# Kernel optimization log

Measured on AMD Instinct MI355X. Metric: run time of the kernel, lower is better.

The kernel has to match this reference:

```python
import jax, jax.numpy as jnp
import numpy as np

HEADS = 4

def cnorm(x):
    # WithBias_LayerNorm over channel dim (no learnable params in source)
    mu = jnp.mean(x, axis=1, keepdims=True)
    var = jnp.mean((x - mu) ** 2, axis=1, keepdims=True)
    return (x - mu) / jnp.sqrt(var + 1e-5)

def conv1x1(x, w):  # w: (O, C)
    return jnp.einsum('bchw,oc->bohw', x, w)

def dwconv(x, w, pad, dil):
    return jax.lax.conv_general_dilated(
        x, w, (1, 1), [(pad, pad), (pad, pad)], rhs_dilation=(dil, dil),
        dimension_numbers=('NCHW', 'OIHW', 'NCHW'), feature_group_count=x.shape[1])

def pshuffle(x, r=2):  # (b, c*r^2, h, w) -> (b, c, h*r, w*r)
    b, c, h, w = x.shape
    x = x.reshape(b, c // (r * r), r, r, h, w)
    return x.transpose(0, 1, 4, 2, 5, 3).reshape(b, c // (r * r), h * r, w * r)

def punshuffle(x, r=2):  # inverse of pshuffle
    b, c, h, w = x.shape
    x = x.reshape(b, c, h // r, r, w // r, r)
    return x.transpose(0, 1, 3, 5, 2, 4).reshape(b, c * r * r, h // r, w // r)

def l2n(x):  # F.normalize over last dim
    return x / jnp.maximum(jnp.linalg.norm(x, axis=-1, keepdims=True), 1e-12)

def setup_inputs() -> dict:
    key = jax.random.key(0)
    ks = jax.random.split(key, 16)
    B, D, H, W = 2, 192, 128, 128
    HID = 512
    s = 0.02
    return {
        'F_raw': jax.random.normal(ks[0], (B, D, H, W), jnp.float32),
        'F_Y': jax.random.normal(ks[1], (B, D, H, W), jnp.float32),
        'temperature': jnp.ones((HEADS, 1, 1), jnp.float32),
        'w_raw_kv': jax.random.normal(ks[2], (2 * D, D), jnp.float32) * s,
        'w_raw_q': jax.random.normal(ks[3], (D, D), jnp.float32) * s,
        'w_rgb_kv': jax.random.normal(ks[4], (2 * D, D), jnp.float32) * s,
        'w_rgb_q': jax.random.normal(ks[5], (D, D), jnp.float32) * s,
        'w_g1': jax.random.normal(ks[6], (4 * D, 2 * D), jnp.float32) * s,
        'b_g1': jnp.zeros((4 * D,), jnp.float32),
        'w_g2': jax.random.normal(ks[7], (1, 4 * D), jnp.float32) * s,
        'b_g2': jnp.zeros((1,), jnp.float32),
        'w_fc': jax.random.normal(ks[8], (D, D), jnp.float32) * s,
        'b_fc': jnp.zeros((D,), jnp.float32),
        'w_pin': jax.random.normal(ks[9], (2 * HID, D), jnp.float32) * s,
        'w_dw5': jax.random.normal(ks[10], (HID // 4, 1, 5, 5), jnp.float32) * s,
        'w_dwd': jax.random.normal(ks[11], (HID // 4, 1, 3, 3), jnp.float32) * s,
        'w_pout': jax.random.normal(ks[12], (D, HID), jnp.float32) * s,
    }

def reference(F_raw, F_Y, temperature, w_raw_kv, w_raw_q, w_rgb_kv, w_rgb_q,
              w_g1, b_g1, w_g2, b_g2, w_fc, b_fc, w_pin, w_dw5, w_dwd, w_pout):
    Fr = cnorm(F_raw)   # source applies norm_g1 to both inputs
    Fy = cnorm(F_Y)
    b, c, h, w = Fr.shape
    hw, ch = h * w, c // HEADS

    raw_k, raw_v = jnp.split(conv1x1(Fr, w_raw_kv), 2, axis=1)
    raw_q = conv1x1(Fr, w_raw_q)
    rgb_k, rgb_v = jnp.split(conv1x1(Fy, w_rgb_kv), 2, axis=1)
    rgb_q = conv1x1(Fy, w_rgb_q)

    heads = lambda x: x.reshape(b, HEADS, ch, hw)
    raw_q, raw_k, raw_v = heads(raw_q), heads(raw_k), heads(raw_v)
    rgb_q, rgb_k, rgb_v = heads(rgb_q), heads(rgb_k), heads(rgb_v)
    raw_q, raw_k = l2n(raw_q), l2n(raw_k)
    rgb_q, rgb_k = l2n(rgb_q), l2n(rgb_k)

    attn_raw = jax.nn.softmax(jnp.einsum('bhcn,bhdn->bhcd', rgb_q, raw_k) * temperature, axis=-1)
    attn_rgb = jax.nn.softmax(jnp.einsum('bhcn,bhdn->bhcd', raw_q, rgb_k) * temperature, axis=-1)
    out_raw = jnp.einsum('bhcd,bhdn->bhcn', attn_raw, raw_v)
    out_rgb = jnp.einsum('bhcd,bhdn->bhcn', attn_rgb, rgb_v)

    fused = jnp.concatenate([Fr, Fy], axis=1)
    g = jax.nn.gelu(conv1x1(fused, w_g1) + b_g1[None, :, None, None], approximate=False)
    alpha = jax.nn.sigmoid(conv1x1(g, w_g2) + b_g2[None, :, None, None])  # (b,1,h,w)
    alpha = alpha.reshape(b, 1, 1, hw)

    context = (alpha * out_raw + (1.0 - alpha) * out_rgb).reshape(b, c, h, w)
    out = conv1x1(context, w_fc) + b_fc[None, :, None, None] + Fr + Fy

    # FeedForward
    x = conv1x1(cnorm(out), w_pin)        # (b, 2*hid, h, w)
    x = pshuffle(x)                       # (b, hid/2, 2h, 2w)
    x1, x2 = jnp.split(x, 2, axis=1)      # (b, hid/4, 2h, 2w) each
    x1 = dwconv(x1, w_dw5, pad=2, dil=1)
    x2 = dwconv(x2, w_dwd, pad=2, dil=2)
    x = (x2 * jnp.tanh(jax.nn.softplus(x2))) * x1  # mish(x2) * x1
    x = punshuffle(x)                     # (b, hid, h, w)
    return out + conv1x1(x, w_pout)
```

## Files before the change

kernel.cpp:

```cpp
#include <hip/hip_runtime.h>
#include <cstdint>
#include <cstddef>


typedef _Float16 f16;
using half8  = __attribute__((ext_vector_type(8))) _Float16;
using float4v = __attribute__((ext_vector_type(4))) float;

#define HW    16384
#define NPIX  32768

union U4H8 { uint4 u; f16 h[8]; };
union U2H4 { uint2 u; f16 h[4]; };

struct WConvArgs { const float* src[7]; f16* dst[7]; int n[7]; };
__global__ __launch_bounds__(256) void wconv_kernel(WConvArgs a) {
  int t = blockIdx.y;
  const float* s = a.src[t]; f16* d = a.dst[t]; int n = a.n[t];
  for (int i = blockIdx.x * 256 + threadIdx.x; i < n; i += gridDim.x * 256)
    d[i] = (f16)s[i];
}

__global__ __launch_bounds__(256) void cnorm_in_kernel(const float* __restrict__ x,
                                                       f16* __restrict__ fcat, int zoff) {
  __shared__ float tile[64][193];
  __shared__ float rsum[64][4], rsq[64][4], mm[64], rr[64];
  int tid = threadIdx.x;
  int P0 = blockIdx.x * 64;
  int b  = P0 >> 14;
  int p0 = P0 & (HW - 1);
  for (int i = tid; i < 64 * 192; i += 256) {
    int c = i >> 6, pp = i & 63;
    tile[pp][c] = x[((size_t)(b * 192 + c)) * HW + p0 + pp];
  }
  __syncthreads();
  {
    int pp = tid >> 2, q = tid & 3;
    float s = 0.f, s2 = 0.f;
    for (int c = q * 48; c < q * 48 + 48; c++) { float v = tile[pp][c]; s += v; s2 += v * v; }
    rsum[pp][q] = s; rsq[pp][q] = s2;
  }
  __syncthreads();
  if (tid < 64) {
    float s  = rsum[tid][0] + rsum[tid][1] + rsum[tid][2] + rsum[tid][3];
    float s2 = rsq[tid][0] + rsq[tid][1] + rsq[tid][2] + rsq[tid][3];
    float mu = s * (1.f / 192.f);
    float var = s2 * (1.f / 192.f) - mu * mu;
    mm[tid] = mu; rr[tid] = rsqrtf(var + 1e-5f);
  }
  __syncthreads();
  for (int i = tid; i < 64 * 192; i += 256) {
    int pp = i / 192, c = i - pp * 192;
    float v = (tile[pp][c] - mm[pp]) * rr[pp];
    fcat[(size_t)(P0 + pp) * 384 + zoff + c] = (f16)v;
  }
}

__global__ __launch_bounds__(256) void norm_pm_kernel(const float* __restrict__ xpm,
                                                      f16* __restrict__ outn) {
  __shared__ float tile[64][193];
  __shared__ float rsum[64][4], rsq[64][4], mm[64], rr[64];
  int tid = threadIdx.x;
  int P0 = blockIdx.x * 64;
  for (int i = tid; i < 64 * 192; i += 256) {
    int pp = i / 192, c = i - pp * 192;
    tile[pp][c] = xpm[(size_t)(P0 + pp) * 192 + c];
  }
  __syncthreads();
  {
    int pp = tid >> 2, q = tid & 3;
    float s = 0.f, s2 = 0.f;
    for (int c = q * 48; c < q * 48 + 48; c++) { float v = tile[pp][c]; s += v; s2 += v * v; }
    rsum[pp][q] = s; rsq[pp][q] = s2;
  }
  __syncthreads();
  if (tid < 64) {
    float s  = rsum[tid][0] + rsum[tid][1] + rsum[tid][2] + rsum[tid][3];
    float s2 = rsq[tid][0] + rsq[tid][1] + rsq[tid][2] + rsq[tid][3];
    float mu = s * (1.f / 192.f);
    float var = s2 * (1.f / 192.f) - mu * mu;
    mm[tid] = mu; rr[tid] = rsqrtf(var + 1e-5f);
  }
  __syncthreads();
  for (int i = tid; i < 64 * 192; i += 256) {
    int pp = i / 192, c = i - pp * 192;
    outn[(size_t)(P0 + pp) * 192 + c] = (f16)((tile[pp][c] - mm[pp]) * rr[pp]);
  }
}

struct G2Args {
  const f16* A; long lda; long aoff;
  const f16* B1; const f16* B2; int b1rows; int Nout; int K; long bStride;
  f16* outH; long ldo;
  const float* bfc; const f16* fcat; float* outpm;
  const float* bg1; const float* wg2; float* alpha_acc;
  const f16* vraw; const f16* vrgb; const float* alpha_pre; const float* bg2;
  const float* outpm_r; float* dout;
};

#define GEMM_SMEM_BYTES 33280

template <int MODE>
__device__ __forceinline__ void gemm2_body(const G2Args& g, int bx, int by, char* smem) {
  f16 (*As)[64] = (f16(*)[64])smem;
  f16 (*Bs)[64] = (f16(*)[64])(smem + 16384);
  float* salpha = (float*)(smem + 32768);

  int tid = threadIdx.x;
  int P0 = by * 128;
  int n0 = bx * 128;
  int wave = tid >> 6, lane = tid & 63, l15 = lane & 15, quad = lane >> 4;
  int m_off = (wave >> 1) * 64, n_off = (wave & 1) * 64;
  int lrow = lane >> 3, loct = lane & 7;
  const f16* B1 = g.B1 + (size_t)(P0 >> 14) * g.bStride;

  f16 hsa[4], hsb[4];
  if (MODE == 2) {
    if (tid < 128) {
      float a = g.alpha_pre[P0 + tid] + g.bg2[0];
      salpha[tid] = 1.f / (1.f + __expf(-a));
    }
    __syncthreads();
#pragma unroll
    for (int i = 0; i < 4; i++) {
      float s0 = salpha[m_off + i * 16 + l15];
      hsa[i] = (f16)s0; hsb[i] = (f16)(1.f - s0);
    }
  }

  float4v acc[4][4];
#pragma unroll
  for (int i = 0; i < 4; i++)
#pragma unroll
    for (int j = 0; j < 4; j++) acc[i][j] = (float4v){0.f, 0.f, 0.f, 0.f};

  int nkt = g.K >> 6;
  for (int kt = 0; kt < nkt; kt++) {
    int k0 = kt << 6;
#pragma unroll
    for (int j = 0; j < 4; j++) {
      int rbase = wave * 32 + j * 8;
      int r = rbase + lrow;
      int oct = loct ^ (r & 7);
      const f16* ga;
      if (MODE == 2) {
        const f16* base = (k0 < 192) ? (g.vraw + 192 + k0) : (g.vrgb + k0);
        ga = base + (size_t)(P0 + r) * 576 + oct * 8;
      } else {
        ga = g.A + (size_t)(P0 + r) * g.lda + g.aoff + k0 + oct * 8;
      }
      __builtin_amdgcn_global_load_lds((const __attribute__((address_space(1))) void*)ga,
                                       (__attribute__((address_space(3))) void*)&As[rbase][0],
                                       16, 0, 0);
    }
#pragma unroll
    for (int j = 0; j < 4; j++) {
      int rbase = wave * 32 + j * 8;
      int r = rbase + lrow;
      int oct = loct ^ (r & 7);
      int n = n0 + r;
      int nc = (n >= g.Nout) ? (g.Nout - 1) : n;
      const f16* gb = (nc < g.b1rows)
                          ? (B1 + (size_t)nc * g.K + k0 + oct * 8)
                          : (g.B2 + (size_t)(nc - g.b1rows) * g.K + k0 + oct * 8);
      __builtin_amdgcn_global_load_lds((const __attribute__((address_space(1))) void*)gb,
                                       (__attribute__((address_space(3))) void*)&Bs[rbase][0],
                                       16, 0, 0);
    }
    __syncthreads();
#pragma unroll
    for (int ks = 0; ks < 2; ks++) {
      half8 af[4], bf[4];
#pragma unroll
      for (int i = 0; i < 4; i++) {
        int ra = m_off + i * 16 + l15;
        af[i] = *(const half8*)&As[ra][(((ks * 4 + quad) ^ (l15 & 7))) * 8];
        int rb = n_off + i * 16 + l15;
        bf[i] = *(const half8*)&Bs[rb][(((ks * 4 + quad) ^ (l15 & 7))) * 8];
      }
      if (MODE == 2) {
#pragma unroll
        for (int i = 0; i < 4; i++) {
          f16 s = (k0 < 192) ? hsa[i] : hsb[i];
          half8 sv = {s, s, s, s, s, s, s, s};
          af[i] *= sv;
        }
      }
#pragma unroll
      for (int mi = 0; mi < 4; mi++)
#pragma unroll
        for (int ni = 0; ni < 4; ni++)
          acc[mi][ni] = __builtin_amdgcn_mfma_f32_16x16x32_f16(af[mi], bf[ni], acc[mi][ni], 0, 0, 0);
    }
    __syncthreads();
  }

  if (MODE == 0) {
#pragma unroll
    for (int mi = 0; mi < 4; mi++) {
      int row = P0 + m_off + mi * 16 + quad * 4;
#pragma unroll
      for (int ni = 0; ni < 4; ni++) {
        int gcol = n0 + n_off + ni * 16 + l15;
        if (gcol < g.Nout) {
#pragma unroll
          for (int r = 0; r < 4; r++)
            g.outH[(size_t)(row + r) * g.ldo + gcol] = (f16)acc[mi][ni][r];
        }
      }
    }
  } else if (MODE == 1) {
    float bg[4], wg[4];
#pragma unroll
    for (int ni = 0; ni < 4; ni++) {
      int gcol = n0 + n_off + ni * 16 + l15;
      bg[ni] = g.bg1[gcol]; wg[ni] = g.wg2[gcol];
    }
    float psum[4][4];
#pragma unroll
    for (int mi = 0; mi < 4; mi++)
#pragma unroll
      for (int r = 0; r < 4; r++) psum[mi][r] = 0.f;
#pragma unroll
    for (int mi = 0; mi < 4; mi++)
#pragma unroll
      for (int ni = 0; ni < 4; ni++)
#pragma unroll
        for (int r = 0; r < 4; r++) {
          float xx = acc[mi][ni][r] + bg[ni];
          float z = 0.7978845608f * (xx + 0.044715f * xx * xx * xx);
          float zc = fminf(fmaxf(z, -10.f), 10.f);
          float t = __expf(2.f * zc);
          float th = (t - 1.f) * __builtin_amdgcn_rcpf(t + 1.f);
          float ge = 0.5f * xx * (1.f + th);
          psum[mi][r] += ge * wg[ni];
        }
#pragma unroll
    for (int s = 1; s < 16; s <<= 1)
#pragma unroll
      for (int mi = 0; mi < 4; mi++)
#pragma unroll
        for (int r = 0; r < 4; r++) psum[mi][r] += __shfl_xor(psum[mi][r], s, 64);
    if (l15 == 0) {
#pragma unroll
      for (int mi = 0; mi < 4; mi++)
#pragma unroll
        for (int r = 0; r < 4; r++)
          atomicAdd(&g.alpha_acc[P0 + m_off + mi * 16 + quad * 4 + r], psum[mi][r]);
    }
  } else if (MODE == 2) {
#pragma unroll
    for (int mi = 0; mi < 4; mi++) {
      int prow = P0 + m_off + mi * 16 + quad * 4;
#pragma unroll
      for (int ni = 0; ni < 4; ni++) {
        int gcol = n0 + n_off + ni * 16 + l15;
        if (gcol < 192) {
#pragma unroll
          for (int r = 0; r < 4; r++) {
            size_t P = (size_t)(prow + r);
            float v = acc[mi][ni][r] + g.bfc[gcol] +
                      (float)g.fcat[P * 384 + gcol] + (float)g.fcat[P * 384 + 192 + gcol];
            g.outpm[P * 192 + gcol] = v;
          }
        }
      }
    }
  } else {
#pragma unroll
    for (int mi = 0; mi < 4; mi++) {
      int prow = P0 + m_off + mi * 16 + quad * 4;
#pragma unroll
      for (int ni = 0; ni < 4; ni++) {
        int gcol = n0 + n_off + ni * 16 + l15;
        if (gcol < 192) {
#pragma unroll
          for (int r = 0; r < 4; r++)
            acc[mi][ni][r] += g.outpm_r[(size_t)(prow + r) * 192 + gcol];
        }
      }
    }
    float (*bounce)[129] = (float(*)[129])smem;
    for (int cg = 0; cg < 4; cg++) {
      __syncthreads();
      if ((wave & 1) == (cg >> 1)) {
#pragma unroll
        for (int nn = 0; nn < 2; nn++) {
          int ni = (cg & 1) * 2 + nn;
          int lc = nn * 16 + l15;
#pragma unroll
          for (int mi = 0; mi < 4; mi++)
#pragma unroll
            for (int r = 0; r < 4; r++)
              bounce[lc][m_off + mi * 16 + quad * 4 + r] = acc[mi][ni][r];
        }
      }
      __syncthreads();
      int c = tid >> 3, ps = (tid & 7) * 16;
      int gc = n0 + cg * 32 + c;
      if (gc < 192) {
        int b = P0 >> 14, p = (P0 & (HW - 1)) + ps;
        float* dst = g.dout + ((size_t)b * 192 + gc) * HW + p;
#pragma unroll
        for (int i = 0; i < 16; i++) dst[i] = bounce[c][ps + i];
      }
    }
  }
}

template <int MODE>
__global__ __launch_bounds__(256) void gemm2_k(G2Args g) {
  __shared__ __align__(16) char smem[GEMM_SMEM_BYTES];
  gemm2_body<MODE>(g, (int)blockIdx.y, (int)blockIdx.x, smem);
}

__global__ __launch_bounds__(256) void gemm_fused_kernel(G2Args j0, G2Args j1, G2Args j2) {
  __shared__ __align__(16) char smem[GEMM_SMEM_BYTES];
  int id = blockIdx.x;
  if (id < 1280)      gemm2_body<0>(j0, id / 256, id & 255, smem);
  else if (id < 2560) gemm2_body<0>(j1, (id - 1280) / 256, id & 255, smem);
  else                gemm2_body<1>(j2, (id - 2560) / 256, id & 255, smem);
}

__global__ __launch_bounds__(256) void qk_transpose_kernel(const f16* __restrict__ qkvR,
                                                           const f16* __restrict__ qkvG,
                                                           f16* __restrict__ qkT) {
  __shared__ f16 T[64][264];
  int tid = threadIdx.x;
  int p0 = blockIdx.x * 256;
  int g  = blockIdx.y;
  int t  = blockIdx.z >> 1, b = blockIdx.z & 1;
  const f16* src = t ? qkvG : qkvR;
  int col0 = (g < 3) ? g * 64 : g * 64 + 192;
#pragma unroll
  for (int i = 0; i < 4; i++) {
    int idx = i * 256 + tid;
    int pp = idx >> 3, c8 = (idx & 7) * 8;
    const f16* s0 = src + ((size_t)(b * HW + p0 + 2 * pp)) * 576 + col0 + c8;
    uint4 v0 = *(const uint4*)s0;
    uint4 v1 = *(const uint4*)(s0 + 576);
    const unsigned* a = (const unsigned*)&v0;
    const unsigned* c = (const unsigned*)&v1;
#pragma unroll
    for (int w = 0; w < 4; w++) {
      unsigned lo = (a[w] & 0xffffu) | (c[w] << 16);
      unsigned hi = (a[w] >> 16) | (c[w] & 0xffff0000u);
      *(unsigned*)&T[c8 + 2 * w][2 * pp]     = lo;
      *(unsigned*)&T[c8 + 2 * w + 1][2 * pp] = hi;
    }
  }
  __syncthreads();
  size_t obase = ((size_t)(t * 2 + b) * 384 + g * 64) * 16384 + p0;
#pragma unroll
  for (int i = 0; i < 8; i++) {
    int idx = i * 256 + tid;
    int row = idx >> 5, p8 = (idx & 31) * 8;
    *(uint4*)(qkT + obase + (size_t)row * 16384 + p8) = *(const uint4*)&T[row][p8];
  }
}

__global__ __launch_bounds__(256) void gram_mfma_kernel(const f16* __restrict__ qkT,
                                                        float* __restrict__ gram) {
  __shared__ __align__(16) f16 As[48][136];
  __shared__ __align__(16) f16 Bs[48][136];
  __shared__ float Gacc[48][49];
  int tid = threadIdx.x;
  int chunk = blockIdx.x;
  int h = blockIdx.y >> 1, pair = blockIdx.y & 1;
  int b = blockIdx.z;
  int tA = pair ? 0 : 1, tB = pair ? 1 : 0;
  const f16* Abase = qkT + ((size_t)(tA * 2 + b) * 384 + 192 + 48 * h) * 16384;
  const f16* Bbase = qkT + ((size_t)(tB * 2 + b) * 384 + 48 * h) * 16384;
  for (int i = tid; i < 48 * 49; i += 256) ((float*)Gacc)[i] = 0.f;
  int wave = tid >> 6, lane = tid & 63, l15 = lane & 15, quad = lane >> 4;
  float4v acc[3][3];
#pragma unroll
  for (int i = 0; i < 3; i++)
#pragma unroll
    for (int j = 0; j < 3; j++) acc[i][j] = (float4v){0.f, 0.f, 0.f, 0.f};
  float ns_acc = 0.f;
  int nrow = tid >> 1, nhalf = tid & 1;

  for (int stage = 0; stage < 8; stage++) {
    int k0 = chunk * 1024 + stage * 128;
    uint4 v[6];
#pragma unroll
    for (int i = 0; i < 6; i++) {
      int idx = i * 256 + tid;
      int row = idx >> 4, seg = (idx & 15) * 8;
      const f16* p = (row < 48) ? (Abase + (size_t)row * 16384 + k0 + seg)
                                : (Bbase + (size_t)(row - 48) * 16384 + k0 + seg);
      v[i] = *(const uint4*)p;
    }
    __syncthreads();
#pragma unroll
    for (int i = 0; i < 6; i++) {
      int idx = i * 256 + tid;
      int row = idx >> 4, seg = (idx & 15) * 8;
      f16* dst = (row < 48) ? &As[row][seg] : &Bs[row - 48][seg];
      *(uint4*)dst = v[i];
    }
    __syncthreads();
    int kk = wave * 32;
    half8 af[3], bf[3];
#pragma unroll
    for (int i = 0; i < 3; i++) {
      af[i] = *(const half8*)&As[i * 16 + l15][kk + quad * 8];
      bf[i] = *(const half8*)&Bs[i * 16 + l15][kk + quad * 8];
    }
#pragma unroll
    for (int mi = 0; mi < 3; mi++)
#pragma unroll
      for (int ni = 0; ni < 3; ni++)
        acc[mi][ni] = __builtin_amdgcn_mfma_f32_16x16x32_f16(af[mi], bf[ni], acc[mi][ni], 0, 0, 0);
    if (tid < 192) {
      const f16* r = (nrow < 48) ? &As[nrow][nhalf * 64] : &Bs[nrow - 48][nhalf * 64];
#pragma unroll
      for (int e = 0; e < 8; e++) {
        U4H8 tt; tt.u = *(const uint4*)(r + e * 8);
#pragma unroll
        for (int j = 0; j < 8; j++) { float x = (float)tt.h[j]; ns_acc += x * x; }
      }
    }
  }
  __syncthreads();
  for (int w = 0; w < 4; w++) {
    if (wave == w) {
#pragma unroll
      for (int mi = 0; mi < 3; mi++)
#pragma unroll
        for (int ni = 0; ni < 3; ni++)
#pragma unroll
          for (int r = 0; r < 4; r++)
            Gacc[mi * 16 + quad * 4 + r][ni * 16 + l15] += acc[mi][ni][r];
    }
    __syncthreads();
  }
  float* base = gram + ((size_t)b * 4 + h) * 4800;
  float* G = base + pair * 2304;
  for (int i = tid; i < 2304; i += 256)
    atomicAdd(G + i, Gacc[i / 48][i - (i / 48) * 48]);
  if (tid < 192) {
    int slot = pair * 2 + (nrow >= 48 ? 1 : 0);
    int ch = (nrow >= 48) ? (nrow - 48) : nrow;
    atomicAdd(base + 4608 + slot * 48 + ch, ns_acc);
  }
}

__global__ void softmax_kernel(const float* __restrict__ gram, const float* __restrict__ temp,
                               float* __restrict__ att) {
  int id = blockIdx.x;
  int b = id >> 3, h = (id >> 1) & 3, pr = id & 1;
  int tid = threadIdx.x;
  __shared__ float srk[48];
  const float* base = gram + ((size_t)b * 4 + h) * 4800;
  const float* G  = base + pr * 2304;
  const float* nq = base + 4608 + (pr ? 96 : 0);
  const float* nk = base + 4608 + (pr ? 144 : 48);
  if (tid < 48) srk[tid] = 1.f / fmaxf(sqrtf(nk[tid]), 1e-12f);
  __syncthreads();
  if (tid < 48) {
    float rq = 1.f / fmaxf(sqrtf(nq[tid]), 1e-12f);
    float T = temp[h];
    float s[48], mx = -1e30f;
#pragma unroll
    for (int d = 0; d < 48; d++) { s[d] = T * G[tid * 48 + d] * rq * srk[d]; mx = fmaxf(mx, s[d]); }
    float sum = 0.f;
#pragma unroll
    for (int d = 0; d < 48; d++) { s[d] = __expf(s[d] - mx); sum += s[d]; }
    float inv = 1.f / sum;
    float* A = att + (((size_t)b * 2 + pr) * 4 + h) * 2304 + tid * 48;
#pragma unroll
    for (int d = 0; d < 48; d++) A[d] = s[d] * inv;
  }
}

__global__ __launch_bounds__(256) void mbuild_kernel(const float* __restrict__ wfc,
                                                     const float* __restrict__ att,
                                                     f16* __restrict__ mcat) {
  int e = blockIdx.x * 256 + threadIdx.x;
  if (e >= 147456) return;
  int b = e / 73728, r = e - b * 73728;
  int o = r / 384, j = r - o * 384;
  int pr = j / 192, jj = j - pr * 192;
  int h = jj / 48, d = jj - h * 48;
  const float* A = att + (((size_t)b * 2 + pr) * 4 + h) * 2304 + d;
  const float* w = wfc + o * 192 + h * 48;
  float s = 0.f;
  for (int c = 0; c < 48; c++) s += w[c] * A[c * 48];
  mcat[(size_t)b * 73728 + o * 384 + j] = (f16)s;
}

__global__ __launch_bounds__(256) void dwmish_kernel(const f16* __restrict__ hid,
                                                     const float* __restrict__ w5,
                                                     const float* __restrict__ w3,
                                                     f16* __restrict__ u) {
  __shared__ f16 sx[324][8];
  int tid = threadIdx.x;
  int c = blockIdx.y, b = blockIdx.z;
  int ti0 = (blockIdx.x >> 3) * 16, tj0 = (blockIdx.x & 7) * 16;
  const float* wp5 = w5 + c * 25;
  const float* wp3 = w3 + c * 9;
  for (int pix = tid; pix < 324; pix += 256) {
    int pi = pix / 18, pj = pix - pi * 18;
    int gi = ti0 - 1 + pi, gj = tj0 - 1 + pj;
    uint2 v0 = {0u, 0u}, v1 = {0u, 0u};
    if (gi >= 0 && gi < 128 && gj >= 0 && gj < 128) {
      const f16* base = hid + ((size_t)b * HW + gi * 128 + gj) * 1024 + c * 4;
      v0 = *(const uint2*)base;
      v1 = *(const uint2*)(base + 512);
    }
    uint4 vv = {v0.x, v0.y, v1.x, v1.y};
    *(uint4*)&sx[pix][0] = vv;
  }
  __syncthreads();
  int ti = tid >> 4, tj = tid & 15;
  U4H8 px[3][3];
#pragma unroll
  for (int dy = 0; dy < 3; dy++)
#pragma unroll
    for (int dx = 0; dx < 3; dx++)
      px[dy][dx].u = *(const uint4*)&sx[(ti + dy) * 18 + tj + dx][0];
  float xf[3][3][8];
#pragma unroll
  for (int dy = 0; dy < 3; dy++)
#pragma unroll
    for (int dx = 0; dx < 3; dx++)
#pragma unroll
      for (int e = 0; e < 8; e++) xf[dy][dx][e] = (float)px[dy][dx].h[e];
  U2H4 res;
#pragma unroll
  for (int pq = 0; pq < 4; pq++) {
    int p = pq >> 1, q = pq & 1;
    float a2 = 0.f;
#pragma unroll
    for (int ky = 0; ky < 3; ky++)
#pragma unroll
      for (int kx = 0; kx < 3; kx++)
        a2 += wp3[ky * 3 + kx] * xf[ky][kx][4 + pq];
    float a1 = 0.f;
#pragma unroll
    for (int dy = -2; dy <= 2; dy++)
#pragma unroll
      for (int dx = -2; dx <= 2; dx++) {
        int s = p + dy, t2 = q + dx;
        int di = s >> 1, ps_ = s & 1;
        int dj = t2 >> 1, qs_ = t2 & 1;
        a1 += wp5[(dy + 2) * 5 + dx + 2] * xf[1 + di][1 + dj][ps_ * 2 + qs_];
      }
    float t = __expf(fminf(a2, 20.f));
    float num = t * (t + 2.f);
    float m = a2 * num * __builtin_amdgcn_rcpf(num + 2.f);
    res.h[pq] = (f16)(m * a1);
  }
  int gi = ti0 + ti, gj = tj0 + tj;
  *(uint2*)(u + ((size_t)b * HW + gi * 128 + gj) * 512 + c * 4) = res.u;
}

extern "C" void kernel_launch(void* const* d_in, const int* in_sizes, int n_in,
                              void* d_out, int out_size, void* d_ws, size_t ws_size,
                              hipStream_t stream) {
  const float* F_raw    = (const float*)d_in[0];
  const float* F_Y      = (const float*)d_in[1];
  const float* temp     = (const float*)d_in[2];
  const float* w_raw_kv = (const float*)d_in[3];
  const float* w_raw_q  = (const float*)d_in[4];
  const float* w_rgb_kv = (const float*)d_in[5];
  const float* w_rgb_q  = (const float*)d_in[6];
  const float* w_g1     = (const float*)d_in[7];
  const float* b_g1     = (const float*)d_in[8];
  const float* w_g2     = (const float*)d_in[9];
  const float* b_g2     = (const float*)d_in[10];
  const float* w_fc     = (const float*)d_in[11];
  const float* b_fc     = (const float*)d_in[12];
  const float* w_pin    = (const float*)d_in[13];
  const float* w_dw5    = (const float*)d_in[14];
  const float* w_dwd    = (const float*)d_in[15];
  const float* w_pout   = (const float*)d_in[16];
  char* ws = (char*)d_ws;
  float* dout = (float*)d_out;

  const size_t O_FCAT  = 0;
  const size_t O_QKV0  = 25165824;
  const size_t O_QKV1  = 62914560;
  const size_t O_ALPHA = 100663296;
  const size_t O_GRAM  = 100794368;
  const size_t O_ATT   = 100947968;
  const size_t O_MCAT  = 101095424;
  const size_t O_WB    = 101390336;
  const size_t O_OUTPM = 103012352;
  const size_t O_QKT   = 103012352;
  const size_t O_NORM  = 128178176;
  const size_t O_HID   = O_QKV0;
  const size_t O_U     = 140761088;
  if (ws_size < 174315520) return;

  f16* wb      = (f16*)(ws + O_WB);
  f16* wb_kvR  = wb;
  f16* wb_qR   = wb + 73728;
  f16* wb_kvG  = wb + 110592;
  f16* wb_qG   = wb + 184320;
  f16* wb_g1   = wb + 221184;
  f16* wb_pin  = wb + 516096;
  f16* wb_pout = wb + 712704;

  WConvArgs wa;
  wa.src[0] = w_raw_kv; wa.dst[0] = wb_kvR;  wa.n[0] = 73728;
  wa.src[1] = w_raw_q;  wa.dst[1] = wb_qR;   wa.n[1] = 36864;
  wa.src[2] = w_rgb_kv; wa.dst[2] = wb_kvG;  wa.n[2] = 73728;
  wa.src[3] = w_rgb_q;  wa.dst[3] = wb_qG;   wa.n[3] = 36864;
  wa.src[4] = w_g1;     wa.dst[4] = wb_g1;   wa.n[4] = 294912;
  wa.src[5] = w_pin;    wa.dst[5] = wb_pin;  wa.n[5] = 196608;
  wa.src[6] = w_pout;   wa.dst[6] = wb_pout; wa.n[6] = 98304;
  wconv_kernel<<<dim3(16, 7), 256, 0, stream>>>(wa);

  hipMemsetAsync(ws + O_ALPHA, 0, 131072 + 153600, stream);

  f16* fcat = (f16*)(ws + O_FCAT);
  cnorm_in_kernel<<<512, 256, 0, stream>>>(F_raw, fcat, 0);
  cnorm_in_kernel<<<512, 256, 0, stream>>>(F_Y, fcat, 192);

  {
    G2Args j0 = {}, j1 = {}, j2 = {};
    j0.A = fcat; j0.lda = 384; j0.aoff = 0;
    j0.B1 = wb_kvR; j0.B2 = wb_qR; j0.b1rows = 384; j0.Nout = 576; j0.K = 192; j0.bStride = 0;
    j0.outH = (f16*)(ws + O_QKV0); j0.ldo = 576;
    j1 = j0;
    j1.aoff = 192; j1.B1 = wb_kvG; j1.B2 = wb_qG; j1.outH = (f16*)(ws + O_QKV1);
    j2.A = fcat; j2.lda = 384; j2.aoff = 0;
    j2.B1 = wb_g1; j2.B2 = wb_g1; j2.b1rows = 768; j2.Nout = 768; j2.K = 384; j2.bStride = 0;
    j2.bg1 = b_g1; j2.wg2 = w_g2; j2.alpha_acc = (float*)(ws + O_ALPHA);
    gemm_fused_kernel<<<4096, 256, 0, stream>>>(j0, j1, j2);
  }
  qk_transpose_kernel<<<dim3(64, 6, 4), 256, 0, stream>>>((const f16*)(ws + O_QKV0),
                                                          (const f16*)(ws + O_QKV1),
                                                          (f16*)(ws + O_QKT));
  gram_mfma_kernel<<<dim3(16, 8, 2), 256, 0, stream>>>((const f16*)(ws + O_QKT),
                                                       (float*)(ws + O_GRAM));
  softmax_kernel<<<16, 64, 0, stream>>>((const float*)(ws + O_GRAM), temp, (float*)(ws + O_ATT));
  mbuild_kernel<<<576, 256, 0, stream>>>(w_fc, (const float*)(ws + O_ATT), (f16*)(ws + O_MCAT));
  {
    G2Args a = {};
    a.B1 = (const f16*)(ws + O_MCAT); a.B2 = (const f16*)(ws + O_MCAT);
    a.b1rows = 192; a.Nout = 192; a.K = 384; a.bStride = 73728;
    a.vraw = (const f16*)(ws + O_QKV0); a.vrgb = (const f16*)(ws + O_QKV1);
    a.alpha_pre = (float*)(ws + O_ALPHA); a.bg2 = b_g2;
    a.bfc = b_fc; a.fcat = fcat; a.outpm = (float*)(ws + O_OUTPM);
    gemm2_k<2><<<dim3(256, 2), 256, 0, stream>>>(a);
  }
  norm_pm_kernel<<<512, 256, 0, stream>>>((const float*)(ws + O_OUTPM), (f16*)(ws + O_NORM));
  {
    G2Args a = {};
    a.A = (const f16*)(ws + O_NORM); a.lda = 192; a.aoff = 0;
    a.B1 = wb_pin; a.B2 = wb_pin; a.b1rows = 1024; a.Nout = 1024; a.K = 192; a.bStride = 0;
    a.outH = (f16*)(ws + O_HID); a.ldo = 1024;
    gemm2_k<0><<<dim3(256, 8), 256, 0, stream>>>(a);
  }
  dwmish_kernel<<<dim3(64, 128, 2), 256, 0, stream>>>((const f16*)(ws + O_HID), w_dw5, w_dwd,
                                                      (f16*)(ws + O_U));
  {
    G2Args a = {};
    a.A = (const f16*)(ws + O_U); a.lda = 512; a.aoff = 0;
    a.B1 = wb_pout; a.B2 = wb_pout; a.b1rows = 192; a.Nout = 192; a.K = 512; a.bStride = 0;
    a.outpm_r = (const float*)(ws + O_OUTPM); a.dout = dout;
    gemm2_k<3><<<dim3(256, 2), 256, 0, stream>>>(a);
  }
}
```

Measured before the change: 446.0 us.

## Split gram reduction into per-chunk partials reduced in softmax kernel

The gram kernel now uses 32 K-chunks instead of 16, doubling the grid to 512 blocks. Each block writes its partial 48x48 Gram tile and partial row norms to a scratch buffer instead of issuing atomicAdds. The softmax kernel, now launched with 256 threads, sums the 32 partials itself before normalizing. This removes atomic contention and the memset of the gram buffer, but adds extra global traffic and a serial 32-way reduction in only 16 softmax blocks.

```diff
diff --git a/kernel.cpp b/kernel.cpp
--- a/kernel.cpp
+++ b/kernel.cpp
@@ -359,8 +359,9 @@
   }
 }
 
-__global__ __launch_bounds__(256) void gram_mfma_kernel(const f16* __restrict__ qkT,
-                                                        float* __restrict__ gram) {
+__global__ __launch_bounds__(256) void gram_partial_kernel(const f16* __restrict__ qkT,
+                                                           float* __restrict__ part,
+                                                           float* __restrict__ npart) {
   __shared__ __align__(16) f16 As[48][136];
   __shared__ __align__(16) f16 Bs[48][136];
   __shared__ float Gacc[48][49];
@@ -373,6 +374,7 @@
   const f16* Bbase = qkT + ((size_t)(tB * 2 + b) * 384 + 48 * h) * 16384;
   for (int i = tid; i < 48 * 49; i += 256) ((float*)Gacc)[i] = 0.f;
   int wave = tid >> 6, lane = tid & 63, l15 = lane & 15, quad = lane >> 4;
+  int rpart = tid >> 4, seg = (tid & 15) * 8;
   float4v acc[3][3];
 #pragma unroll
   for (int i = 0; i < 3; i++)
@@ -381,13 +383,12 @@
   float ns_acc = 0.f;
   int nrow = tid >> 1, nhalf = tid & 1;
 
-  for (int stage = 0; stage < 8; stage++) {
-    int k0 = chunk * 1024 + stage * 128;
+  for (int stage = 0; stage < 4; stage++) {
+    int k0 = chunk * 512 + stage * 128;
     uint4 v[6];
 #pragma unroll
     for (int i = 0; i < 6; i++) {
-      int idx = i * 256 + tid;
-      int row = idx >> 4, seg = (idx & 15) * 8;
+      int row = i * 16 + rpart;
       const f16* p = (row < 48) ? (Abase + (size_t)row * 16384 + k0 + seg)
                                 : (Bbase + (size_t)(row - 48) * 16384 + k0 + seg);
       v[i] = *(const uint4*)p;
@@ -395,8 +396,7 @@
     __syncthreads();
 #pragma unroll
     for (int i = 0; i < 6; i++) {
-      int idx = i * 256 + tid;
-      int row = idx >> 4, seg = (idx & 15) * 8;
+      int row = i * 16 + rpart;
       f16* dst = (row < 48) ? &As[row][seg] : &Bs[row - 48][seg];
       *(uint4*)dst = v[i];
     }
@@ -436,31 +436,48 @@
     }
     __syncthreads();
   }
-  float* base = gram + ((size_t)b * 4 + h) * 4800;
-  float* G = base + pair * 2304;
+  int id = b * 8 + h * 2 + pair;
+  float* P = part + ((size_t)id * 32 + chunk) * 2304;
   for (int i = tid; i < 2304; i += 256)
-    atomicAdd(G + i, Gacc[i / 48][i - (i / 48) * 48]);
+    P[i] = Gacc[i / 48][i - (i / 48) * 48];
   if (tid < 192) {
-    int slot = pair * 2 + (nrow >= 48 ? 1 : 0);
-    int ch = (nrow >= 48) ? (nrow - 48) : nrow;
-    atomicAdd(base + 4608 + slot * 48 + ch, ns_acc);
-  }
-}
-
-__global__ void softmax_kernel(const float* __restrict__ gram, const float* __restrict__ temp,
-                               float* __restrict__ att) {
+    float tot = ns_acc + __shfl_xor(ns_acc, 1, 64);
+    if (nhalf == 0) {
+      int slot = pair * 2 + (nrow >= 48 ? 1 : 0);
+      int ch = (nrow >= 48) ? (nrow - 48) : nrow;
+      npart[((size_t)((b * 4 + h) * 4 + slot) * 32 + chunk) * 48 + ch] = tot;
+    }
+  }
+}
+
+__global__ __launch_bounds__(256) void softmax_kernel(const float* __restrict__ part,
+                                                      const float* __restrict__ npart,
+                                                      const float* __restrict__ temp,
+                                                      float* __restrict__ att) {
+  __shared__ float G[2304];
+  __shared__ float srq[48], srk[48];
   int id = blockIdx.x;
   int b = id >> 3, h = (id >> 1) & 3, pr = id & 1;
   int tid = threadIdx.x;
-  __shared__ float srk[48];
-  const float* base = gram + ((size_t)b * 4 + h) * 4800;
-  const float* G  = base + pr * 2304;
-  const float* nq = base + 4608 + (pr ? 96 : 0);
-  const float* nk = base + 4608 + (pr ? 144 : 48);
-  if (tid < 48) srk[tid] = 1.f / fmaxf(sqrtf(nk[tid]), 1e-12f);
+  const float* P = part + (size_t)id * 32 * 2304;
+  for (int i = tid; i < 2304; i += 256) {
+    float s = 0.f;
+    for (int c = 0; c < 32; c++) s += P[(size_t)c * 2304 + i];
+    G[i] = s;
+  }
+  if (tid < 96) {
+    int isk = tid >= 48;
+    int ch = isk ? tid - 48 : tid;
+    int slot = pr * 2 + isk;
+    const float* NP = npart + (size_t)((b * 4 + h) * 4 + slot) * 32 * 48;
+    float s = 0.f;
+    for (int c = 0; c < 32; c++) s += NP[c * 48 + ch];
+    float r = 1.f / fmaxf(sqrtf(s), 1e-12f);
+    if (isk) srk[ch] = r; else srq[ch] = r;
+  }
   __syncthreads();
   if (tid < 48) {
-    float rq = 1.f / fmaxf(sqrtf(nq[tid]), 1e-12f);
+    float rq = srq[tid];
     float T = temp[h];
     float s[48], mx = -1e30f;
 #pragma unroll
@@ -584,7 +601,6 @@
   const size_t O_QKV0  = 25165824;
   const size_t O_QKV1  = 62914560;
   const size_t O_ALPHA = 100663296;
-  const size_t O_GRAM  = 100794368;
   const size_t O_ATT   = 100947968;
   const size_t O_MCAT  = 101095424;
   const size_t O_WB    = 101390336;
@@ -593,6 +609,8 @@
   const size_t O_NORM  = 128178176;
   const size_t O_HID   = O_QKV0;
   const size_t O_U     = 140761088;
+  const size_t O_PART  = 153344000;
+  const size_t O_NPART = 158062592;
   if (ws_size < 174315520) return;
 
   f16* wb      = (f16*)(ws + O_WB);
@@ -614,7 +632,7 @@
   wa.src[6] = w_pout;   wa.dst[6] = wb_pout; wa.n[6] = 98304;
   wconv_kernel<<<dim3(16, 7), 256, 0, stream>>>(wa);
 
-  hipMemsetAsync(ws + O_ALPHA, 0, 131072 + 153600, stream);
+  hipMemsetAsync(ws + O_ALPHA, 0, 131072, stream);
 
   f16* fcat = (f16*)(ws + O_FCAT);
   cnorm_in_kernel<<<512, 256, 0, stream>>>(F_raw, fcat, 0);
@@ -635,9 +653,12 @@
   qk_transpose_kernel<<<dim3(64, 6, 4), 256, 0, stream>>>((const f16*)(ws + O_QKV0),
                                                           (const f16*)(ws + O_QKV1),
                                                           (f16*)(ws + O_QKT));
-  gram_mfma_kernel<<<dim3(16, 8, 2), 256, 0, stream>>>((const f16*)(ws + O_QKT),
-                                                       (float*)(ws + O_GRAM));
-  softmax_kernel<<<16, 64, 0, stream>>>((const float*)(ws + O_GRAM), temp, (float*)(ws + O_ATT));
+  gram_partial_kernel<<<dim3(32, 8, 2), 256, 0, stream>>>((const f16*)(ws + O_QKT),
+                                                          (float*)(ws + O_PART),
+                                                          (float*)(ws + O_NPART));
+  softmax_kernel<<<16, 256, 0, stream>>>((const float*)(ws + O_PART),
+                                         (const float*)(ws + O_NPART),
+                                         temp, (float*)(ws + O_ATT));
   mbuild_kernel<<<576, 256, 0, stream>>>(w_fc, (const float*)(ws + O_ATT), (f16*)(ws + O_MCAT));
   {
     G2Args a = {};
```

After: 458.2 us. 1.03x slower.
